# Performance work log

Measured on AMD Instinct MI355X. Metric: run time of the kernel, lower is better.

Reference implementation:

```python
import jax, jax.numpy as jnp
import numpy as np
import math

DIM = 1024
NH = 16
HD = DIM // NH
SEQ = 2048
B = 2
P = 16
HIDDEN = 2816  # multiple_of*ceil(int(2*4*dim/3)/multiple_of)


def justnorm(x, axis=-1):
    n = jnp.sqrt(jnp.sum(x * x, axis=axis, keepdims=True))
    return x / jnp.maximum(n, 1e-12)


def adafm_modulate(x, ftime, p):
    # x: [B,H,W]; ftime: [B, p*p] real
    Bb, H, W = x.shape
    xp = x.reshape(Bb, H // p, p, W // p, p).transpose(0, 1, 3, 2, 4).reshape(Bb, H // p, W // p, p * p)
    fspec = jnp.fft.fft2(xp)  # over last two axes (W//p, p*p)
    fspec = fspec * ftime.reshape(Bb, 1, 1, p * p)
    fout = jnp.fft.ifft2(fspec).real
    fout = fout.reshape(Bb, H // p, W // p, p, p).transpose(0, 1, 3, 2, 4).reshape(Bb, H, W)
    return fout


def apply_rotary(xq, xk, cos, sin):
    # xq,xk: [B,S,NH,HD]; cos,sin: [S, HD//2]
    def rot(t):
        tr = t.reshape(*t.shape[:-1], HD // 2, 2)
        a, b = tr[..., 0], tr[..., 1]
        c = cos[None, :, None, :]
        s = sin[None, :, None, :]
        ra = a * c - b * s
        rb = a * s + b * c
        return jnp.stack([ra, rb], axis=-1).reshape(t.shape)
    return rot(xq), rot(xk)


def attention(x, cos, sin, wq, wk, wv, wo, sqk):
    bsz, seqlen, _ = x.shape
    xq = (x @ wq).reshape(bsz, seqlen, NH, HD)
    xk = (x @ wk).reshape(bsz, seqlen, NH, HD)
    xv = (x @ wv).reshape(bsz, seqlen, NH, HD)
    xq, xk = apply_rotary(xq, xk, cos, sin)
    sqk_eff = (sqk * math.sqrt(DIM)).reshape(1, 1, NH, HD)  # sqk_init_value/sqk_init_scaling = sqrt(dim)
    xq = sqk_eff * justnorm(xq)
    xk = sqk_eff * justnorm(xk)
    scale = HD ** 0.5
    scores = jnp.einsum('bqhd,bkhd->bhqk', xq, xk) * scale
    attn = jax.nn.softmax(scores, axis=-1)
    out = jnp.einsum('bhqk,bkhd->bqhd', attn, xv).reshape(bsz, seqlen, DIM)
    return out @ wo


def feed_forward(x, w1, w2, w3, su, sv):
    x1 = x @ w1
    x3 = x @ w3
    scale = math.sqrt(HIDDEN)
    h = jax.nn.silu(x1 * sv * scale) * (x3 * su)
    return h @ w2


def setup_inputs() -> dict:
    key = jax.random.key(0)
    ks = jax.random.split(key, 12)
    inv = 1.0 / (10000.0 ** (np.arange(0, HD, 2, dtype=np.float32) / HD))
    ang = np.outer(np.arange(SEQ, dtype=np.float32), inv)
    s = 0.02
    return {
        'x': jax.random.normal(ks[0], (B, SEQ, DIM), jnp.float32),
        'freqs_cos': jnp.asarray(np.cos(ang), jnp.float32),
        'freqs_sin': jnp.asarray(np.sin(ang), jnp.float32),
        'adafm_input': jax.random.normal(ks[1], (B, DIM), jnp.float32),
        'wq': jax.random.normal(ks[2], (DIM, DIM), jnp.float32) * s,
        'wk': jax.random.normal(ks[3], (DIM, DIM), jnp.float32) * s,
        'wv': jax.random.normal(ks[4], (DIM, DIM), jnp.float32) * s,
        'wo': jax.random.normal(ks[5], (DIM, DIM), jnp.float32) * s,
        'sqk': jnp.full((DIM,), 1.0 / math.sqrt(DIM), jnp.float32),
        'w1': jax.random.normal(ks[6], (DIM, HIDDEN), jnp.float32) * s,
        'w2': jax.random.normal(ks[7], (HIDDEN, DIM), jnp.float32) * s,
        'w3': jax.random.normal(ks[8], (DIM, HIDDEN), jnp.float32) * s,
        'su': jnp.ones((HIDDEN,), jnp.float32),
        'sv': jnp.ones((HIDDEN,), jnp.float32),
        'proj_w': jax.random.normal(ks[9], (DIM, 2 * P * P), jnp.float32) * s,
        'proj_b': jnp.zeros((2 * P * P,), jnp.float32),
        'attn_alpha': jnp.full((DIM,), 0.05 / math.sqrt(DIM), jnp.float32),
        'mlp_alpha': jnp.full((DIM,), 0.05 / math.sqrt(DIM), jnp.float32),
    }


def reference(x, freqs_cos, freqs_sin, adafm_input, wq, wk, wv, wo, sqk, w1, w2, w3, su, sv, proj_w, proj_b, attn_alpha, mlp_alpha):
    # AdaFM projection: SiLU -> Linear
    t = jax.nn.silu(adafm_input) @ proj_w + proj_b  # [B, 2*P*P]
    msa_time, mlp_time = t[:, :P * P], t[:, P * P:]

    alpha_scale = 0.05 * math.sqrt(DIM)  # attn_alpha_init_value / attn_alpha_init_scaling
    lr = jnp.abs(attn_alpha * alpha_scale)
    h = justnorm(x)
    h_a = attention(adafm_modulate(x, msa_time, P), freqs_cos, freqs_sin, wq, wk, wv, wo, sqk)
    h_a = justnorm(h_a)
    x = justnorm(h + lr * (h_a - h))

    lr = jnp.abs(mlp_alpha * alpha_scale)
    h = justnorm(x)
    h_m = feed_forward(adafm_modulate(x, mlp_time, P), w1, w2, w3, su, sv)
    h_m = justnorm(h_m)
    x = justnorm(h + lr * (h_m - h))
    return x
```

## Files before the change

### kernel.cpp

```cpp
#include <hip/hip_runtime.h>
#include <hip/hip_bf16.h>
#include <math.h>

#define SEQ    2048
#define DIMN   1024
#define NHEAD  16
#define HDIM   64
#define BATCH  2
#define ROWS   4096
#define HIDDEN 2816
#define QKVS   3072

typedef __attribute__((ext_vector_type(8))) short short8;
typedef __attribute__((ext_vector_type(4))) float f32x4;
typedef unsigned short ushort_t;
typedef __attribute__((address_space(1))) void gas_t;
typedef __attribute__((address_space(3))) void las_t;

__device__ __forceinline__ float bfbits(ushort_t u){ return __uint_as_float(((unsigned)u) << 16); }
__device__ __forceinline__ ushort_t f2bu(float f){
  __hip_bfloat16 h = __float2bfloat16(f);
  return *reinterpret_cast<ushort_t*>(&h);
}
__device__ __forceinline__ ushort_t f2bu_t(float f){ return (ushort_t)(__float_as_uint(f) >> 16); }
__device__ __forceinline__ float ldv(const float* p){ return *p; }
__device__ __forceinline__ float ldv(const ushort_t* p){ return bfbits(*p); }
__device__ __forceinline__ void stv(float* p, float v){ *p = v; }
__device__ __forceinline__ void stv(ushort_t* p, float v){ *p = f2bu(v); }
__device__ __forceinline__ void async_cp16(const ushort_t* g, ushort_t* l){
  __builtin_amdgcn_global_load_lds((gas_t*)g, (las_t*)l, 16, 0, 0);
}
__device__ __forceinline__ ushort4 ld4u(const float* p){
  float4 v = *(const float4*)p;
  ushort4 u; u.x = f2bu(v.x); u.y = f2bu(v.y); u.z = f2bu(v.z); u.w = f2bu(v.w);
  return u;
}
__device__ __forceinline__ ushort4 ld4u(const ushort_t* p){ return *(const ushort4*)p; }

__global__ void k_time(const float* __restrict__ ada, const float* __restrict__ pw,
                       const float* __restrict__ pb, float* __restrict__ t){
  int b = blockIdx.x >> 9, o = blockIdx.x & 511, lane = threadIdx.x;
  float acc = 0.f;
  for(int i = lane; i < DIMN; i += 64){
    float a = ada[b*DIMN + i];
    float s = a / (1.f + expf(-a));
    acc += s * pw[i*512 + o];
  }
  for(int off = 32; off; off >>= 1) acc += __shfl_down(acc, off);
  if(lane == 0) t[b*512 + o] = acc + pb[o];
}

__global__ void k_gp(const float* __restrict__ t, ushort_t* __restrict__ Gpk){
  __shared__ float gl[256];
  int wb = blockIdx.x, kc = blockIdx.y, tid = threadIdx.x;
  int b = wb & 1, which = wb >> 1;
  const float C = 6.283185307179586f / 256.f;
  float acc = 0.f;
  for(int k = 0; k < 256; k++){
    float f = t[b*512 + which*256 + k];
    acc += f * cosf(C * (float)((k*tid) & 255));
  }
  gl[tid] = acc * (1.f/256.f);
  __syncthreads();
  ushort_t* ob = Gpk + ((size_t)(wb*8 + kc))*8192;
  for(int rep = 0; rep < 4; rep++){
    int n = rep*64 + (tid >> 2), mmb = (tid & 3)*8;
    short8 o;
    #pragma unroll
    for(int j = 0; j < 8; j++)
      o[j] = (short)f2bu(gl[(n - kc*32 - (mmb + j)) & 255]);
    *(short8*)(ob + n*32 + mmb) = o;
  }
}

#define APAD 264
#define GPAD 40
template<typename IN>
__global__ __launch_bounds__(256) void k_modmf(const IN* __restrict__ src,
        const ushort_t* __restrict__ Gpk, ushort_t* __restrict__ dst){
  __shared__ __align__(16) ushort_t Ap[64*APAD];
  __shared__ __align__(16) ushort_t Gs[128*GPAD];
  int nh = blockIdx.x, i = blockIdx.y, b = blockIdx.z;
  int tid = threadIdx.x, lane = tid & 63, w = tid >> 6;
  int l15 = lane & 15, quad = lane >> 4;
  const IN* xb = src + (size_t)b*SEQ*DIMN + (size_t)(i*16)*DIMN;
  int j = tid >> 2, c = (tid & 3)*4;
  #pragma unroll 4
  for(int rep = 0; rep < 16; rep++){
    ushort4 v4 = ld4u(xb + (size_t)rep*DIMN + tid*4);
    *(ushort4*)&Ap[j*APAD + rep*16 + c] = v4;
  }
  f32x4 acc[8];
  #pragma unroll
  for(int nt = 0; nt < 8; nt++){ acc[nt][0]=0.f; acc[nt][1]=0.f; acc[nt][2]=0.f; acc[nt][3]=0.f; }
  for(int kc = 0; kc < 8; kc++){
    __syncthreads();
    {
      const ushort_t* gsrc = Gpk + ((size_t)(b*8 + kc))*8192 + nh*4096;
      #pragma unroll
      for(int r2 = 0; r2 < 2; r2++){
        int n = r2*64 + (tid >> 2), mm = (tid & 3)*8;
        *(short8*)&Gs[n*GPAD + mm] = *(const short8*)(gsrc + r2*2048 + tid*8);
      }
    }
    __syncthreads();
    short8 af = *(const short8*)&Ap[(w*16 + l15)*APAD + kc*32 + quad*8];
    #pragma unroll
    for(int nt = 0; nt < 8; nt++){
      short8 bf = *(const short8*)&Gs[(nt*16 + l15)*GPAD + quad*8];
      acc[nt] = __builtin_amdgcn_mfma_f32_16x16x32_bf16(af, bf, acc[nt], 0, 0, 0);
    }
  }
  size_t ob = (size_t)b*SEQ*DIMN + (size_t)(i*16 + nh*8)*DIMN + (w*16 + quad*4)*16 + l15;
  #pragma unroll
  for(int nt = 0; nt < 8; nt++)
    #pragma unroll
    for(int t = 0; t < 4; t++)
      dst[ob + (size_t)nt*DIMN + t*16] = f2bu(acc[nt][t]);
}

struct WtJob { const float* src; ushort_t* dst; int K, N, nx, tstart; };
struct WtJobs { WtJob j[7]; };
__global__ __launch_bounds__(256) void k_wtall(WtJobs jobs){
  __shared__ float tile[32][33];
  int bid = blockIdx.x;
  int ji = 0;
  #pragma unroll
  for(int i = 1; i < 7; i++) if(bid >= jobs.j[i].tstart) ji = i;
  const float* W = jobs.j[ji].src;
  ushort_t* Wt = jobs.j[ji].dst;
  int K = jobs.j[ji].K, N = jobs.j[ji].N;
  int tt = bid - jobs.j[ji].tstart;
  int n0 = (tt % jobs.j[ji].nx)*32, k0 = (tt / jobs.j[ji].nx)*32;
  int r = threadIdx.x >> 3, c4 = (threadIdx.x & 7)*4;
  float4 v = *(const float4*)(W + (size_t)(k0 + r)*N + n0 + c4);
  tile[r][c4+0] = v.x; tile[r][c4+1] = v.y; tile[r][c4+2] = v.z; tile[r][c4+3] = v.w;
  __syncthreads();
  ushort4 o;
  o.x = f2bu(tile[c4+0][r]); o.y = f2bu(tile[c4+1][r]);
  o.z = f2bu(tile[c4+2][r]); o.w = f2bu(tile[c4+3][r]);
  *(ushort4*)(Wt + (size_t)(n0 + r)*K + k0 + c4) = o;
}

template<int BM, int BN, typename OUT>
__global__ __launch_bounds__(256) void k_gemm_mf(const ushort_t* __restrict__ A,
        const ushort_t* __restrict__ Wt, OUT* __restrict__ C, int N, int K){
  constexpr int MT = BM/32, NT = BN/32;
  constexpr int AI = BM/64, BI = BN/64;
  __shared__ __align__(16) ushort_t As[BM*32];
  __shared__ __align__(16) ushort_t Bs[BN*32];
  int tid = threadIdx.x, lane = tid & 63, w = tid >> 6;
  int l15 = lane & 15, quad = lane >> 4;
  int m0 = blockIdx.y*BM, n0 = blockIdx.x*BN;
  int wr = (w>>1)*(BM/2), wc = (w&1)*(BN/2);
  int srow = lane >> 2, scol = (lane & 3)*8;
  const ushort_t* ag[AI]; ushort_t* al[AI];
  const ushort_t* bg[BI]; ushort_t* bl[BI];
  #pragma unroll
  for(int i = 0; i < AI; i++){
    int rb = w*AI + i;
    ag[i] = A + (size_t)(m0 + rb*16 + srow)*K + scol;
    al[i] = As + rb*512 + lane*8;
  }
  #pragma unroll
  for(int i = 0; i < BI; i++){
    int rb = w*BI + i;
    bg[i] = Wt + (size_t)(n0 + rb*16 + srow)*K + scol;
    bl[i] = Bs + rb*512 + lane*8;
  }
  f32x4 acc[MT][NT];
  #pragma unroll
  for(int mt = 0; mt < MT; mt++)
    #pragma unroll
    for(int nt = 0; nt < NT; nt++)
      for(int t = 0; t < 4; t++) acc[mt][nt][t] = 0.f;
  for(int kk = 0; kk < K; kk += 32){
    __syncthreads();
    #pragma unroll
    for(int i = 0; i < AI; i++) async_cp16(ag[i] + kk, al[i]);
    #pragma unroll
    for(int i = 0; i < BI; i++) async_cp16(bg[i] + kk, bl[i]);
    __syncthreads();
    short8 af[MT], bf[NT];
    #pragma unroll
    for(int mt = 0; mt < MT; mt++) af[mt] = *(const short8*)&As[(wr + mt*16 + l15)*32 + quad*8];
    #pragma unroll
    for(int nt = 0; nt < NT; nt++) bf[nt] = *(const short8*)&Bs[(wc + nt*16 + l15)*32 + quad*8];
    #pragma unroll
    for(int mt = 0; mt < MT; mt++)
      #pragma unroll
      for(int nt = 0; nt < NT; nt++)
        acc[mt][nt] = __builtin_amdgcn_mfma_f32_16x16x32_bf16(af[mt], bf[nt], acc[mt][nt], 0, 0, 0);
  }
  #pragma unroll
  for(int mt = 0; mt < MT; mt++)
    #pragma unroll
    for(int nt = 0; nt < NT; nt++)
      #pragma unroll
      for(int t = 0; t < 4; t++)
        stv(C + (size_t)(m0 + wr + mt*16 + quad*4 + t)*N + n0 + wc + nt*16 + l15, acc[mt][nt][t]);
}

__global__ __launch_bounds__(256) void k_ffn12(const ushort_t* __restrict__ A,
        const ushort_t* __restrict__ W1t, const ushort_t* __restrict__ W3t,
        const float* __restrict__ su, const float* __restrict__ sv,
        ushort_t* __restrict__ H, int K){
  __shared__ __align__(16) ushort_t As[128*32];
  __shared__ __align__(16) ushort_t B1s[64*32];
  __shared__ __align__(16) ushort_t B3s[64*32];
  int tid = threadIdx.x, lane = tid & 63, w = tid >> 6;
  int l15 = lane & 15, quad = lane >> 4;
  int m0 = blockIdx.y*128, n0 = blockIdx.x*64;
  int wr = (w>>1)*64, wc = (w&1)*32;
  int srow = lane >> 2, scol = (lane & 3)*8;
  const ushort_t* ag[2]; ushort_t* al[2];
  #pragma unroll
  for(int i = 0; i < 2; i++){
    int rb = w*2 + i;
    ag[i] = A + (size_t)(m0 + rb*16 + srow)*K + scol;
    al[i] = As + rb*512 + lane*8;
  }
  const ushort_t* b1g = W1t + (size_t)(n0 + w*16 + srow)*K + scol;
  const ushort_t* b3g = W3t + (size_t)(n0 + w*16 + srow)*K + scol;
  ushort_t* b1l = B1s + w*512 + lane*8;
  ushort_t* b3l = B3s + w*512 + lane*8;
  f32x4 acc1[4][2], acc3[4][2];
  #pragma unroll
  for(int mt = 0; mt < 4; mt++)
    #pragma unroll
    for(int nt = 0; nt < 2; nt++)
      for(int t = 0; t < 4; t++){ acc1[mt][nt][t] = 0.f; acc3[mt][nt][t] = 0.f; }
  for(int kk = 0; kk < K; kk += 32){
    __syncthreads();
    async_cp16(ag[0] + kk, al[0]);
    async_cp16(ag[1] + kk, al[1]);
    async_cp16(b1g + kk, b1l);
    async_cp16(b3g + kk, b3l);
    __syncthreads();
    short8 af[4], b1f[2], b3f[2];
    #pragma unroll
    for(int mt = 0; mt < 4; mt++) af[mt] = *(const short8*)&As[(wr + mt*16 + l15)*32 + quad*8];
    #pragma unroll
    for(int nt = 0; nt < 2; nt++){
      b1f[nt] = *(const short8*)&B1s[(wc + nt*16 + l15)*32 + quad*8];
      b3f[nt] = *(const short8*)&B3s[(wc + nt*16 + l15)*32 + quad*8];
    }
    #pragma unroll
    for(int mt = 0; mt < 4; mt++)
      #pragma unroll
      for(int nt = 0; nt < 2; nt++){
        acc1[mt][nt] = __builtin_amdgcn_mfma_f32_16x16x32_bf16(af[mt], b1f[nt], acc1[mt][nt], 0, 0, 0);
        acc3[mt][nt] = __builtin_amdgcn_mfma_f32_16x16x32_bf16(af[mt], b3f[nt], acc3[mt][nt], 0, 0, 0);
      }
  }
  #pragma unroll
  for(int nt = 0; nt < 2; nt++){
    int n = n0 + wc + nt*16 + l15;
    float svv = sv[n] * 53.06599665f, suv = su[n];
    #pragma unroll
    for(int mt = 0; mt < 4; mt++)
      #pragma unroll
      for(int t = 0; t < 4; t++){
        float hpre = acc1[mt][nt][t] * svv;
        float sil = hpre / (1.f + expf(-hpre));
        float hv = sil * (acc3[mt][nt][t] * suv);
        H[(size_t)(m0 + wr + mt*16 + quad*4 + t)*HIDDEN + n] = f2bu(hv);
      }
  }
}

__global__ __launch_bounds__(256) void k_qkvt(ushort_t* __restrict__ qkv,
        ushort_t* __restrict__ vto, const float* __restrict__ fc,
        const float* __restrict__ fs, const float* __restrict__ sqk){
  __shared__ ushort_t tile[64][72];
  int s0 = blockIdx.x*64, h = blockIdx.y, b = blockIdx.z;
  int tid = threadIdx.x;
  int r = tid >> 2, c = (tid & 3)*16;
  const ushort_t* vsrc = qkv + (size_t)(b*SEQ + s0 + r)*QKVS + 2048 + h*HDIM + c;
  *(short8*)&tile[r][c]     = *(const short8*)vsrc;
  *(short8*)&tile[r][c + 8] = *(const short8*)(vsrc + 8);
  size_t qb_ = (size_t)(b*SEQ + s0 + r)*QKVS + h*HDIM + c;
  short8 q0 = *(const short8*)(qkv + qb_),        q1 = *(const short8*)(qkv + qb_ + 8);
  short8 k0 = *(const short8*)(qkv + qb_ + 1024), k1 = *(const short8*)(qkv + qb_ + 1032);
  int s = s0 + r;
  float qr[16], kr[16];
  float sq = 0.f, sk = 0.f;
  #pragma unroll
  for(int j = 0; j < 16; j += 2){
    float qa = bfbits((ushort_t)(j < 8 ? q0[j] : q1[j-8]));
    float qb2 = bfbits((ushort_t)(j+1 < 8 ? q0[j+1] : q1[j-7]));
    float ka = bfbits((ushort_t)(j < 8 ? k0[j] : k1[j-8]));
    float kb2 = bfbits((ushort_t)(j+1 < 8 ? k0[j+1] : k1[j-7]));
    float co = fc[s*32 + ((c + j) >> 1)], si = fs[s*32 + ((c + j) >> 1)];
    qr[j]   = qa*co - qb2*si;  qr[j+1] = qa*si + qb2*co;
    kr[j]   = ka*co - kb2*si;  kr[j+1] = ka*si + kb2*co;
    sq += qr[j]*qr[j] + qr[j+1]*qr[j+1];
    sk += kr[j]*kr[j] + kr[j+1]*kr[j+1];
  }
  sq += __shfl_xor(sq, 1); sq += __shfl_xor(sq, 2);
  sk += __shfl_xor(sk, 1); sk += __shfl_xor(sk, 2);
  float rq = 1.f / fmaxf(sqrtf(sq), 1e-12f);
  float rk = 1.f / fmaxf(sqrtf(sk), 1e-12f);
  short8 oq0, oq1, ok0, ok1;
  #pragma unroll
  for(int j = 0; j < 8; j++){
    float s0v = sqk[h*HDIM + c + j] * 32.f;
    float s1v = sqk[h*HDIM + c + 8 + j] * 32.f;
    oq0[j] = (short)f2bu(s0v*qr[j]*rq);   oq1[j] = (short)f2bu(s1v*qr[8+j]*rq);
    ok0[j] = (short)f2bu(s0v*kr[j]*rk);   ok1[j] = (short)f2bu(s1v*kr[8+j]*rk);
  }
  *(short8*)(qkv + qb_)        = oq0;  *(short8*)(qkv + qb_ + 8)    = oq1;
  *(short8*)(qkv + qb_ + 1024) = ok0;  *(short8*)(qkv + qb_ + 1032) = ok1;
  __syncthreads();
  ushort_t* dst = vto + ((size_t)(b*NHEAD + h)*HDIM + r)*SEQ + s0 + c;
  for(int j2 = 0; j2 < 16; j2 += 4){
    ushort4 o;
    o.x = tile[c+j2][r]; o.y = tile[c+j2+1][r]; o.z = tile[c+j2+2][r]; o.w = tile[c+j2+3][r];
    *(ushort4*)(dst + j2) = o;
  }
}

#define LSTR 72
__global__ __launch_bounds__(256) void k_flash_mf(const ushort_t* __restrict__ qkv,
        const ushort_t* __restrict__ vt, ushort_t* __restrict__ out){
  int qb = blockIdx.x, h = blockIdx.y, b = blockIdx.z;
  int tid = threadIdx.x, lane = tid & 63, w = tid >> 6;
  int l15 = lane & 15, quad = lane >> 4;
  __shared__ __align__(16) ushort_t Ks[64*LSTR], Vts[64*LSTR];
  __shared__ __align__(16) ushort_t Ps[4][16*LSTR];
  size_t qkb = (size_t)b*SEQ*QKVS + h*HDIM;
  size_t ob  = (size_t)b*SEQ*DIMN + h*HDIM;
  const ushort_t* vb = vt + (size_t)(b*NHEAD + h)*HDIM*SEQ;
  short8 qf0, qf1;
  {
    const ushort_t* qrow = qkv + qkb + (size_t)(qb*64 + w*16 + l15)*QKVS;
    qf0 = *(const short8*)(qrow + quad*8);
    qf1 = *(const short8*)(qrow + 32 + quad*8);
  }
  f32x4 o_acc[4];
  #pragma unroll
  for(int g = 0; g < 4; g++){ o_acc[g][0]=0.f; o_acc[g][1]=0.f; o_acc[g][2]=0.f; o_acc[g][3]=0.f; }
  float lsum = 0.f;
  int sr = tid >> 2, sc = tid & 3;
  const ushort_t* kbase = qkv + qkb + 1024 + (size_t)sr*QKVS + sc*16;
  const ushort_t* vbase = vb + (size_t)sr*SEQ + sc*16;
  short8 kr0 = *(const short8*)kbase, kr1 = *(const short8*)(kbase + 8);
  short8 vr0 = *(const short8*)vbase, vr1 = *(const short8*)(vbase + 8);
  const float C1 = 11.54156036f;
  const float C2 = 11.90223409f;
  for(int ch = 0; ch < SEQ/64; ch++){
    __syncthreads();
    *(short8*)&Ks[sr*LSTR + sc*16]      = kr0;
    *(short8*)&Ks[sr*LSTR + sc*16 + 8]  = kr1;
    *(short8*)&Vts[sr*LSTR + sc*16]     = vr0;
    *(short8*)&Vts[sr*LSTR + sc*16 + 8] = vr1;
    if(ch + 1 < SEQ/64){
      const ushort_t* kn = kbase + (size_t)(ch + 1)*64*QKVS;
      const ushort_t* vn = vbase + (ch + 1)*64;
      kr0 = *(const short8*)kn; kr1 = *(const short8*)(kn + 8);
      vr0 = *(const short8*)vn; vr1 = *(const short8*)(vn + 8);
    }
    __syncthreads();
    #pragma unroll
    for(int g = 0; g < 4; g++){
      f32x4 sa; sa[0]=0.f; sa[1]=0.f; sa[2]=0.f; sa[3]=0.f;
      short8 k0 = *(const short8*)&Ks[(g*16 + l15)*LSTR + quad*8];
      short8 k1 = *(const short8*)&Ks[(g*16 + l15)*LSTR + 32 + quad*8];
      sa = __builtin_amdgcn_mfma_f32_16x16x32_bf16(k0, qf0, sa, 0, 0, 0);
      sa = __builtin_amdgcn_mfma_f32_16x16x32_bf16(k1, qf1, sa, 0, 0, 0);
      float e0 = exp2f(fmaf(sa[0], C1, -C2));
      float e1 = exp2f(fmaf(sa[1], C1, -C2));
      float e2 = exp2f(fmaf(sa[2], C1, -C2));
      float e3 = exp2f(fmaf(sa[3], C1, -C2));
      lsum += (e0 + e1) + (e2 + e3);
      ushort4 pk;
      pk.x = f2bu_t(e0); pk.y = f2bu_t(e1); pk.z = f2bu_t(e2); pk.w = f2bu_t(e3);
      *(ushort4*)&Ps[w][l15*LSTR + g*16 + quad*4] = pk;
    }
    short8 a0 = *(const short8*)&Ps[w][l15*LSTR + quad*8];
    short8 a1 = *(const short8*)&Ps[w][l15*LSTR + 32 + quad*8];
    #pragma unroll
    for(int g = 0; g < 4; g++){
      short8 b0 = *(const short8*)&Vts[(g*16 + l15)*LSTR + quad*8];
      short8 b1 = *(const short8*)&Vts[(g*16 + l15)*LSTR + 32 + quad*8];
      o_acc[g] = __builtin_amdgcn_mfma_f32_16x16x32_bf16(a0, b0, o_acc[g], 0, 0, 0);
      o_acc[g] = __builtin_amdgcn_mfma_f32_16x16x32_bf16(a1, b1, o_acc[g], 0, 0, 0);
    }
  }
  lsum += __shfl_xor(lsum, 16);
  lsum += __shfl_xor(lsum, 32);
  #pragma unroll
  for(int t = 0; t < 4; t++){
    float inv = 1.f / __shfl(lsum, quad*4 + t);
    #pragma unroll
    for(int g = 0; g < 4; g++)
      out[ob + (size_t)(qb*64 + w*16 + quad*4 + t)*DIMN + g*16 + l15] = f2bu(o_acc[g][t] * inv);
  }
}

__device__ __forceinline__ float blockReduceSum(float v, float* red){
  for(int off = 32; off; off >>= 1) v += __shfl_xor(v, off);
  int wid = threadIdx.x >> 6;
  if((threadIdx.x & 63) == 0) red[wid] = v;
  __syncthreads();
  float tot = red[0] + red[1] + red[2] + red[3];
  __syncthreads();
  return tot;
}

template<typename T1, typename T2, typename TO>
__global__ void k_rn(const T1* __restrict__ x, const T2* __restrict__ ha,
        const float* __restrict__ alpha, TO* __restrict__ xo){
  __shared__ float red[4];
  int row = blockIdx.x, tid = threadIdx.x;
  size_t base = (size_t)row * DIMN;
  float xs[4], hs[4], cs[4];
  float s1 = 0.f, s2 = 0.f;
  for(int j = 0; j < 4; j++){
    int i = tid + j*256;
    float xv = ldv(x + base + i);  xs[j] = xv; s1 += xv*xv;
    float hv = ldv(ha + base + i); hs[j] = hv; s2 += hv*hv;
  }
  s1 = blockReduceSum(s1, red);
  s2 = blockReduceSum(s2, red);
  float r1 = 1.f / fmaxf(sqrtf(s1), 1e-12f);
  float r2 = 1.f / fmaxf(sqrtf(s2), 1e-12f);
  float s3 = 0.f;
  for(int j = 0; j < 4; j++){
    int i = tid + j*256;
    float lr = fabsf(alpha[i] * 1.6f);
    float hn = xs[j] * r1;
    float cv = hn + lr*(hs[j]*r2 - hn);
    cs[j] = cv; s3 += cv*cv;
  }
  s3 = blockReduceSum(s3, red);
  float r3 = 1.f / fmaxf(sqrtf(s3), 1e-12f);
  for(int j = 0; j < 4; j++){
    int i = tid + j*256;
    stv(xo + base + i, cs[j] * r3);
  }
}

extern "C" void kernel_launch(void* const* d_in, const int* in_sizes, int n_in,
                              void* d_out, int out_size, void* d_ws, size_t ws_size,
                              hipStream_t stream){
  const float* x   = (const float*)d_in[0];
  const float* fc  = (const float*)d_in[1];
  const float* fs  = (const float*)d_in[2];
  const float* ada = (const float*)d_in[3];
  const float* wq  = (const float*)d_in[4];
  const float* wk  = (const float*)d_in[5];
  const float* wv  = (const float*)d_in[6];
  const float* wo  = (const float*)d_in[7];
  const float* sqk = (const float*)d_in[8];
  const float* w1  = (const float*)d_in[9];
  const float* w2  = (const float*)d_in[10];
  const float* w3  = (const float*)d_in[11];
  const float* su  = (const float*)d_in[12];
  const float* sv  = (const float*)d_in[13];
  const float* pw  = (const float*)d_in[14];
  const float* pb  = (const float*)d_in[15];
  const float* aal = (const float*)d_in[16];
  const float* mal = (const float*)d_in[17];
  float* out = (float*)d_out;

  const size_t MM = (size_t)DIMN*DIMN;
  const size_t HM = (size_t)HIDDEN*DIMN;
  const size_t F  = (size_t)ROWS*DIMN;
  char* wsb = (char*)d_ws;
  float* t = (float*)wsb;
  ushort_t* Gpk = (ushort_t*)(wsb + 16384);
  ushort_t* wqT = Gpk + 262144;
  ushort_t* wkT = wqT + MM;
  ushort_t* wvT = wkT + MM;
  ushort_t* woT = wvT + MM;
  ushort_t* w1T = woT + MM;
  ushort_t* w3T = w1T + HM;
  ushort_t* w2T = w3T + HM;
  ushort_t* P1  = w2T + HM;
  ushort_t* QKV = P1 + F;
  ushort_t* Ha  = QKV;
  ushort_t* M2  = QKV + F;
  ushort_t* Hm  = QKV + 2*F;
  ushort_t* a1  = QKV + 3*F;
  ushort_t* Vt  = a1;

  dim3 blk(256);

  k_time<<<dim3(1024), dim3(64), 0, stream>>>(ada, pw, pb, t);
  k_gp<<<dim3(4,8), blk, 0, stream>>>(t, Gpk);

  WtJobs jobs;
  jobs.j[0] = {wq, wqT, DIMN, DIMN, 32, 0};
  jobs.j[1] = {wk, wkT, DIMN, DIMN, 32, 1024};
  jobs.j[2] = {wv, wvT, DIMN, DIMN, 32, 2048};
  jobs.j[3] = {wo, woT, DIMN, DIMN, 32, 3072};
  jobs.j[4] = {w1, w1T, DIMN, HIDDEN, HIDDEN/32, 4096};
  jobs.j[5] = {w3, w3T, DIMN, HIDDEN, HIDDEN/32, 4096 + 2816};
  jobs.j[6] = {w2, w2T, HIDDEN, DIMN, 32, 4096 + 5632};
  k_wtall<<<dim3(12544), blk, 0, stream>>>(jobs);

  k_modmf<float><<<dim3(2,128,BATCH), blk, 0, stream>>>(x, Gpk, P1);
  k_gemm_mf<128,128,ushort_t><<<dim3(24,32), blk, 0, stream>>>(P1, wqT, QKV, QKVS, DIMN);
  k_qkvt<<<dim3(SEQ/64,NHEAD,BATCH), blk, 0, stream>>>(QKV, Vt, fc, fs, sqk);
  k_flash_mf<<<dim3(SEQ/64,NHEAD,BATCH), blk, 0, stream>>>(QKV, Vt, P1);
  k_gemm_mf<128,64,ushort_t><<<dim3(16,32), blk, 0, stream>>>(P1, woT, Ha, DIMN, DIMN);
  k_rn<float,ushort_t,ushort_t><<<dim3(ROWS), blk, 0, stream>>>(x, Ha, aal, P1);

  k_modmf<ushort_t><<<dim3(2,128,BATCH), blk, 0, stream>>>(P1, Gpk + 131072, M2);
  k_ffn12<<<dim3(HIDDEN/64,ROWS/128), blk, 0, stream>>>(M2, w1T, w3T, su, sv, a1, DIMN);
  k_gemm_mf<128,64,ushort_t><<<dim3(16,32), blk, 0, stream>>>(a1, w2T, Hm, DIMN, HIDDEN);
  k_rn<ushort_t,ushort_t,float><<<dim3(ROWS), blk, 0, stream>>>(P1, Hm, mal, out);
}
```

Measured before the change: 495.7 us.

## Load K and V fragments directly from global memory in flash attention

Result: slower. 631.0 us (+27.3%).

```diff
diff --git a/kernel.cpp b/kernel.cpp
--- a/kernel.cpp
+++ b/kernel.cpp
@@ -326,7 +326,6 @@
   int qb = blockIdx.x, h = blockIdx.y, b = blockIdx.z;
   int tid = threadIdx.x, lane = tid & 63, w = tid >> 6;
   int l15 = lane & 15, quad = lane >> 4;
-  __shared__ __align__(16) ushort_t Ks[64*LSTR], Vts[64*LSTR];
   __shared__ __align__(16) ushort_t Ps[4][16*LSTR];
   size_t qkb = (size_t)b*SEQ*QKVS + h*HDIM;
   size_t ob  = (size_t)b*SEQ*DIMN + h*HDIM;
@@ -341,33 +340,29 @@
   #pragma unroll
   for(int g = 0; g < 4; g++){ o_acc[g][0]=0.f; o_acc[g][1]=0.f; o_acc[g][2]=0.f; o_acc[g][3]=0.f; }
   float lsum = 0.f;
-  int sr = tid >> 2, sc = tid & 3;
-  const ushort_t* kbase = qkv + qkb + 1024 + (size_t)sr*QKVS + sc*16;
-  const ushort_t* vbase = vb + (size_t)sr*SEQ + sc*16;
-  short8 kr0 = *(const short8*)kbase, kr1 = *(const short8*)(kbase + 8);
-  short8 vr0 = *(const short8*)vbase, vr1 = *(const short8*)(vbase + 8);
+  const ushort_t* kb_ = qkv + qkb + 1024;
   const float C1 = 11.54156036f;
   const float C2 = 11.90223409f;
   for(int ch = 0; ch < SEQ/64; ch++){
-    __syncthreads();
-    *(short8*)&Ks[sr*LSTR + sc*16]      = kr0;
-    *(short8*)&Ks[sr*LSTR + sc*16 + 8]  = kr1;
-    *(short8*)&Vts[sr*LSTR + sc*16]     = vr0;
-    *(short8*)&Vts[sr*LSTR + sc*16 + 8] = vr1;
-    if(ch + 1 < SEQ/64){
-      const ushort_t* kn = kbase + (size_t)(ch + 1)*64*QKVS;
-      const ushort_t* vn = vbase + (ch + 1)*64;
-      kr0 = *(const short8*)kn; kr1 = *(const short8*)(kn + 8);
-      vr0 = *(const short8*)vn; vr1 = *(const short8*)(vn + 8);
-    }
-    __syncthreads();
+    short8 kf[4][2];
+    #pragma unroll
+    for(int g = 0; g < 4; g++){
+      const ushort_t* kr = kb_ + (size_t)(ch*64 + g*16 + l15)*QKVS + quad*8;
+      kf[g][0] = *(const short8*)kr;
+      kf[g][1] = *(const short8*)(kr + 32);
+    }
+    short8 vf[4][2];
+    #pragma unroll
+    for(int g = 0; g < 4; g++){
+      const ushort_t* vr = vb + (size_t)(g*16 + l15)*SEQ + ch*64 + quad*8;
+      vf[g][0] = *(const short8*)vr;
+      vf[g][1] = *(const short8*)(vr + 32);
+    }
     #pragma unroll
     for(int g = 0; g < 4; g++){
       f32x4 sa; sa[0]=0.f; sa[1]=0.f; sa[2]=0.f; sa[3]=0.f;
-      short8 k0 = *(const short8*)&Ks[(g*16 + l15)*LSTR + quad*8];
-      short8 k1 = *(const short8*)&Ks[(g*16 + l15)*LSTR + 32 + quad*8];
-      sa = __builtin_amdgcn_mfma_f32_16x16x32_bf16(k0, qf0, sa, 0, 0, 0);
-      sa = __builtin_amdgcn_mfma_f32_16x16x32_bf16(k1, qf1, sa, 0, 0, 0);
+      sa = __builtin_amdgcn_mfma_f32_16x16x32_bf16(kf[g][0], qf0, sa, 0, 0, 0);
+      sa = __builtin_amdgcn_mfma_f32_16x16x32_bf16(kf[g][1], qf1, sa, 0, 0, 0);
       float e0 = exp2f(fmaf(sa[0], C1, -C2));
       float e1 = exp2f(fmaf(sa[1], C1, -C2));
       float e2 = exp2f(fmaf(sa[2], C1, -C2));
@@ -381,10 +376,8 @@
     short8 a1 = *(const short8*)&Ps[w][l15*LSTR + 32 + quad*8];
     #pragma unroll
     for(int g = 0; g < 4; g++){
-      short8 b0 = *(const short8*)&Vts[(g*16 + l15)*LSTR + quad*8];
-      short8 b1 = *(const short8*)&Vts[(g*16 + l15)*LSTR + 32 + quad*8];
-      o_acc[g] = __builtin_amdgcn_mfma_f32_16x16x32_bf16(a0, b0, o_acc[g], 0, 0, 0);
-      o_acc[g] = __builtin_amdgcn_mfma_f32_16x16x32_bf16(a1, b1, o_acc[g], 0, 0, 0);
+      o_acc[g] = __builtin_amdgcn_mfma_f32_16x16x32_bf16(a0, vf[g][0], o_acc[g], 0, 0, 0);
+      o_acc[g] = __builtin_amdgcn_mfma_f32_16x16x32_bf16(a1, vf[g][1], o_acc[g], 0, 0, 0);
     }
   }
   lsum += __shfl_xor(lsum, 16);
```
